# Performance work log

Measured on AMD Instinct MI355X. Metric: run time of the kernel, lower is better.

Reference implementation:

```python
import jax, jax.numpy as jnp
import numpy as np

B, N, D, H = 4, 4096, 1024, 16  # batch, seq_len, d_model, nhead
GN_EPS = 0.00064


def setup_inputs() -> dict:
    key = jax.random.key(0)
    ks = jax.random.split(key, 12)
    x = jax.random.normal(ks[0], (B, N, D), jnp.float32)
    ddd = jnp.linspace(0.0, 1.0, D).reshape(1, 1, D)
    s = 1.0 / np.sqrt(D)  # xavier-ish scale for DxD linears
    w = lambda k: jax.random.normal(k, (D, D), jnp.float32) * s
    return {
        "x": x,
        "x_r": 1.0 - ddd ** 0.2,
        "x_w": 1.0 - ddd ** 0.9,
        "x_k": 1.0 - ddd ** 0.7,
        "x_v": 1.0 - ddd ** 0.7,
        "x_a": 1.0 - ddd ** 0.9,
        "x_g": 1.0 - ddd ** 0.2,
        "W_r": w(ks[1]),   # receptance
        "W_w": w(ks[2]),   # time_decay
        "W_k": w(ks[3]),   # key
        "W_v": w(ks[4]),   # value
        "W_a": w(ks[5]),   # in_context
        "W_g": w(ks[6]),   # gate
        "W_out": jax.random.normal(ks[7], (D, D), jnp.float32) * s,
        "b_out": jax.random.normal(ks[8], (D,), jnp.float32) * 0.01,
        "gn_w": 1.0 + 0.1 * jax.random.normal(ks[9], (D,), jnp.float32),
        "gn_b": 0.1 * jax.random.normal(ks[10], (D,), jnp.float32),
    }


def reference(x, x_r, x_w, x_k, x_v, x_a, x_g,
              W_r, W_w, W_k, W_v, W_a, W_g,
              W_out, b_out, gn_w, gn_b):
    b, n, d = x.shape
    # previous-token shift delta: prev - x, with zero prev at t=0
    prev = jnp.concatenate([jnp.zeros_like(x[:, :1]), x[:, :-1]], axis=1)
    xx = prev - x

    lin = lambda mix, W: (x + xx * mix) @ W.T  # torch Linear: y = z @ W^T
    r = jax.nn.sigmoid(lin(x_r, W_r))
    decay = jnp.exp(-jax.nn.softplus(lin(x_w, W_w)))
    k = jnp.tanh(lin(x_k, W_k))
    v = lin(x_v, W_v)
    alpha = jax.nn.sigmoid(lin(x_a, W_a))
    g = jax.nn.sigmoid(lin(x_g, W_g))

    # per-channel recurrence: state = state * decay_t + alpha_t * k_t * v_t
    u = alpha * k * v  # [B, N, D]
    def step(state, inp):
        d_t, u_t, r_t = inp
        state = state * d_t + u_t
        return state, r_t * state

    inputs_tm = (jnp.swapaxes(decay, 0, 1),  # time-major [N, B, D]
                 jnp.swapaxes(u, 0, 1),
                 jnp.swapaxes(r, 0, 1))
    state0 = jnp.zeros((b, d), x.dtype)
    _, mixed_tm = jax.lax.scan(step, state0, inputs_tm)
    mixed = jnp.swapaxes(mixed_tm, 0, 1)  # [B, N, D]

    # GroupNorm(H groups) over reshaped [B*N, D]
    m = mixed.reshape(b * n, H, d // H)
    mu = m.mean(-1, keepdims=True)
    var = ((m - mu) ** 2).mean(-1, keepdims=True)  # biased, as torch GroupNorm
    mn = ((m - mu) / jnp.sqrt(var + GN_EPS)).reshape(b, n, d)
    mn = mn * gn_w + gn_b

    return (mn * g) @ W_out.T + b_out
```

## Files before the change

kernel.cpp:

```cpp
#include <hip/hip_runtime.h>
#include <cstdint>
#include <cstddef>

#define D_MODEL 1024
#define SEQ_LEN 4096
#define NBATCH  4
#define M_ROWS  (NBATCH * SEQ_LEN)
#define NCHUNK  64
#define CHLEN   64
#define GN_EPS_F 0.00064f

typedef unsigned short u16;
typedef __attribute__((ext_vector_type(4))) float f32x4;
typedef __attribute__((ext_vector_type(8))) __bf16 bf16x8;

enum { ACT_DECAY = 0, ACT_TANH, ACT_VMUL, ACT_U, ACT_SIG, ACT_BIAS, ACT_ID };

__device__ __forceinline__ u16 f2bf(float f) {
  union { float f; uint32_t u; } un; un.f = f;
  uint32_t r = (un.u + 0x7FFFu + ((un.u >> 16) & 1u)) >> 16;
  return (u16)r;
}
__device__ __forceinline__ float bf2f(u16 h) {
  union { uint32_t u; float f; } un; un.u = ((uint32_t)h) << 16;
  return un.f;
}
__device__ __forceinline__ float sigm(float y) { return 1.f / (1.f + expf(-y)); }

__device__ __forceinline__ void load_lds16(const u16* g, u16* l) {
  __builtin_amdgcn_global_load_lds(
      (const __attribute__((address_space(1))) void*)g,
      (__attribute__((address_space(3))) void*)l, 16, 0, 0);
}

__global__ __launch_bounds__(256) void wconv(
    const float* __restrict__ w0, const float* __restrict__ w1,
    const float* __restrict__ w2, const float* __restrict__ w3,
    const float* __restrict__ w4, const float* __restrict__ w5,
    const float* __restrict__ w6, u16* __restrict__ Wb) {
  const int gid = blockIdx.x * 256 + threadIdx.x;
  const int m = gid >> 18;
  const int off = gid & 262143;
  const float* src;
  switch (m) {
    case 0: src = w0; break; case 1: src = w1; break; case 2: src = w2; break;
    case 3: src = w3; break; case 4: src = w4; break; case 5: src = w5; break;
    default: src = w6; break;
  }
  const float4 v = ((const float4*)src)[off];
  ushort4 o;
  o.x = f2bf(v.x); o.y = f2bf(v.y); o.z = f2bf(v.z); o.w = f2bf(v.w);
  ((ushort4*)Wb)[gid] = o;
}

__global__ __launch_bounds__(256) void zgen2(
    const float* __restrict__ x, const float* __restrict__ mixA,
    const float* __restrict__ mixB, u16* __restrict__ zA,
    u16* __restrict__ zB) {
  const int gid = blockIdx.x * 256 + threadIdx.x;
  const int dv = gid & 255;
  const int n = (gid >> 8) & (SEQ_LEN - 1);
  const float4 xv = ((const float4*)x)[gid];
  float4 pv = make_float4(0.f, 0.f, 0.f, 0.f);
  if (n > 0) pv = ((const float4*)x)[gid - 256];
  const float4 dxv = make_float4(pv.x - xv.x, pv.y - xv.y, pv.z - xv.z, pv.w - xv.w);
  const float4 ma = ((const float4*)mixA)[dv];
  const float4 mb = ((const float4*)mixB)[dv];
  ushort4 oa, ob;
  oa.x = f2bf(xv.x + dxv.x * ma.x); ob.x = f2bf(xv.x + dxv.x * mb.x);
  oa.y = f2bf(xv.y + dxv.y * ma.y); ob.y = f2bf(xv.y + dxv.y * mb.y);
  oa.z = f2bf(xv.z + dxv.z * ma.z); ob.z = f2bf(xv.z + dxv.z * mb.z);
  oa.w = f2bf(xv.w + dxv.w * ma.w); ob.w = f2bf(xv.w + dxv.w * mb.w);
  ((ushort4*)zA)[gid] = oa;
  ((ushort4*)zB)[gid] = ob;
}

template <int ACT>
__global__ __launch_bounds__(512, 4) void gemm_bt(
    const u16* __restrict__ A,
    const u16* __restrict__ Bw,
    void* __restrict__ outp,
    const u16* __restrict__ aux,
    const float* __restrict__ bias) {
  __shared__ __align__(16) u16 AL[2][128 * 32];
  __shared__ __align__(16) u16 BL[2][256 * 32];
  const int tid = threadIdx.x;
  const int lane = tid & 63;
  const int wid = tid >> 6;
  const int wr = wid >> 2;
  const int wc = wid & 3;
  const int lr = lane & 15;
  const int lk = lane >> 4;

  const int bid = blockIdx.x;
  const int wgid = (bid & 7) * 64 + (bid >> 3);
  const int m0 = (wgid >> 2) * 128;
  const int n0 = (wgid & 3) * 256;

  const int srow = tid >> 2;
  const int ssw  = ((tid & 3) ^ ((srow >> 1) & 3)) * 8;
  const u16* gA  = A  + (size_t)(m0 + srow) * D_MODEL + ssw;
  const u16* gB0 = Bw + (size_t)(n0 + srow) * D_MODEL + ssw;
  const u16* gB1 = Bw + (size_t)(n0 + 128 + srow) * D_MODEL + ssw;
#define SA(bufi, kt) load_lds16(gA  + (kt), &AL[bufi][wid * 512])
#define SB0(bufi, kt) load_lds16(gB0 + (kt), &BL[bufi][wid * 512])
#define SB1(bufi, kt) load_lds16(gB1 + (kt), &BL[bufi][4096 + wid * 512])

  const int rA = wr * 64;
  const int rB = wc * 64;

  f32x4 acc[4][4];
  const f32x4 z4 = {0.f, 0.f, 0.f, 0.f};
#pragma unroll
  for (int i = 0; i < 4; i++)
#pragma unroll
    for (int j = 0; j < 4; j++) acc[i][j] = z4;

  SB0(0, 0); SB1(0, 0); SA(0, 0);

  int cur = 0;
  for (int t = 0; t < 32; ++t) {
    const int nxt = cur ^ 1;
    const int ktn = (t + 1) * 32;
    const bool more = (t < 31);
    const u16* uA = AL[cur];
    const u16* uB = BL[cur];
    bf16x8 a[4], b[4];

    if (more) { SB0(nxt, ktn); SB1(nxt, ktn); }
    if (more) asm volatile("s_waitcnt vmcnt(2)" ::: "memory");
    else      asm volatile("s_waitcnt vmcnt(0)" ::: "memory");
    __builtin_amdgcn_s_barrier();
    __builtin_amdgcn_sched_barrier(0);
#pragma unroll
    for (int mi = 0; mi < 4; ++mi) {
      const int R = rA + mi * 16 + lr;
      a[mi] = *(const bf16x8*)&uA[R * 32 + ((lk ^ ((R >> 1) & 3)) << 3)];
    }
#pragma unroll
    for (int nj = 0; nj < 4; ++nj) {
      const int R = rB + nj * 16 + lr;
      b[nj] = *(const bf16x8*)&uB[R * 32 + ((lk ^ ((R >> 1) & 3)) << 3)];
    }
    __builtin_amdgcn_s_setprio(1);
#pragma unroll
    for (int mi = 0; mi < 4; ++mi)
#pragma unroll
      for (int nj = 0; nj < 2; ++nj)
        acc[mi][nj] = __builtin_amdgcn_mfma_f32_16x16x32_bf16(a[mi], b[nj], acc[mi][nj], 0, 0, 0);
    __builtin_amdgcn_s_setprio(0);

    if (more) SA(nxt, ktn);
    __builtin_amdgcn_s_barrier();
    __builtin_amdgcn_s_setprio(1);
#pragma unroll
    for (int mi = 0; mi < 4; ++mi)
#pragma unroll
      for (int nj = 2; nj < 4; ++nj)
        acc[mi][nj] = __builtin_amdgcn_mfma_f32_16x16x32_bf16(a[mi], b[nj], acc[mi][nj], 0, 0, 0);
    __builtin_amdgcn_s_setprio(0);
    cur = nxt;
  }
#undef SA
#undef SB0
#undef SB1

#pragma unroll
  for (int mi = 0; mi < 4; ++mi) {
#pragma unroll
    for (int nj = 0; nj < 4; ++nj) {
#pragma unroll
      for (int e = 0; e < 4; ++e) {
        const int row = m0 + wr * 64 + mi * 16 + lk * 4 + e;
        const int col = n0 + wc * 64 + nj * 16 + lr;
        const size_t idx = (size_t)row * D_MODEL + col;
        const float y = acc[mi][nj][e];
        if constexpr (ACT == ACT_ID) {
          ((u16*)outp)[idx] = f2bf(y);
        } else if constexpr (ACT == ACT_TANH) {
          ((u16*)outp)[idx] = f2bf(tanhf(y));
        } else if constexpr (ACT == ACT_VMUL) {
          ((u16*)outp)[idx] = f2bf(y * bf2f(aux[idx]));
        } else if constexpr (ACT == ACT_U) {
          ((u16*)outp)[idx] = f2bf(sigm(y) * bf2f(aux[idx]));
        } else if constexpr (ACT == ACT_SIG) {
          ((u16*)outp)[idx] = f2bf(sigm(y));
        } else {
          ((float*)outp)[idx] = y + bias[col];
        }
      }
    }
  }
}

__global__ __launch_bounds__(256) void scan1(
    const u16* __restrict__ wraw, const u16* __restrict__ u,
    float* __restrict__ Ac, float* __restrict__ Sc) {
  const int gid = blockIdx.x * 256 + threadIdx.x;
  const int d = gid & 1023;
  const int b = (gid >> 10) & 3;
  const int c = gid >> 12;
  const size_t base = ((size_t)b * SEQ_LEN + (size_t)c * CHLEN) * D_MODEL + d;
  float A = 1.f, S = 0.f;
#pragma unroll 4
  for (int t = 0; t < CHLEN; t++) {
    const size_t off = base + (size_t)t * D_MODEL;
    const float dd = 1.f / (1.f + expf(bf2f(wraw[off])));
    S = S * dd + bf2f(u[off]);
    A *= dd;
  }
  Ac[gid] = A;
  Sc[gid] = S;
}

__global__ __launch_bounds__(256) void scan2(
    const float* __restrict__ Ac, const float* __restrict__ Sc,
    float* __restrict__ In) {
  const int gid = blockIdx.x * 256 + threadIdx.x;
  float carry = 0.f;
#pragma unroll 4
  for (int c = 0; c < NCHUNK; c++) {
    const int i = c * 4096 + gid;
    In[i] = carry;
    carry = carry * Ac[i] + Sc[i];
  }
}

__global__ __launch_bounds__(1024) void scan3gn(
    const u16* __restrict__ wraw, const u16* __restrict__ u,
    const u16* __restrict__ r, const u16* __restrict__ g,
    const float* __restrict__ In, const float* __restrict__ gw,
    const float* __restrict__ gb, u16* __restrict__ h) {
  const int d = threadIdx.x;
  const int b = blockIdx.x >> 6;
  const int c = blockIdx.x & 63;
  const size_t base = ((size_t)b * SEQ_LEN + (size_t)c * CHLEN) * D_MODEL + d;
  float state = In[c * 4096 + b * 1024 + d];
  const float w_ = gw[d], bb_ = gb[d];
  for (int t = 0; t < CHLEN; t++) {
    const size_t off = base + (size_t)t * D_MODEL;
    const float dd = 1.f / (1.f + expf(bf2f(wraw[off])));
    state = state * dd + bf2f(u[off]);
    const float mixed = bf2f(r[off]) * state;
    float s = mixed, s2 = mixed * mixed;
#pragma unroll
    for (int m = 32; m > 0; m >>= 1) {
      s += __shfl_xor(s, m, 64);
      s2 += __shfl_xor(s2, m, 64);
    }
    const float mu = s * (1.f / 64.f);
    const float var = s2 * (1.f / 64.f) - mu * mu;
    const float inv = 1.f / sqrtf(var + GN_EPS_F);
    h[off] = f2bf(((mixed - mu) * inv * w_ + bb_) * bf2f(g[off]));
  }
}

extern "C" void kernel_launch(void* const* d_in, const int* in_sizes, int n_in,
                              void* d_out, int out_size, void* d_ws, size_t ws_size,
                              hipStream_t stream) {
  (void)in_sizes; (void)n_in; (void)out_size; (void)ws_size;
  const float* x    = (const float*)d_in[0];
  const float* mx_r = (const float*)d_in[1];
  const float* mx_w = (const float*)d_in[2];
  const float* mx_k = (const float*)d_in[3];
  const float* mx_v = (const float*)d_in[4];
  const float* mx_a = (const float*)d_in[5];
  const float* mx_g = (const float*)d_in[6];
  const float* W_r  = (const float*)d_in[7];
  const float* W_w  = (const float*)d_in[8];
  const float* W_k  = (const float*)d_in[9];
  const float* W_v  = (const float*)d_in[10];
  const float* W_a  = (const float*)d_in[11];
  const float* W_g  = (const float*)d_in[12];
  const float* W_o  = (const float*)d_in[13];
  const float* b_out = (const float*)d_in[14];
  const float* gn_w  = (const float*)d_in[15];
  const float* gn_b  = (const float*)d_in[16];

  char* ws = (char*)d_ws;
  const size_t MB = 1024ull * 1024ull;
  u16*   Wb   = (u16*)(ws);
  float* Ac   = (float*)(ws + 14 * MB);
  float* Sc   = (float*)(ws + 15 * MB);
  u16*   z1   = (u16*)(ws + 16 * MB);
  u16*   z2   = (u16*)(ws + 48 * MB);
  u16*   wraw = (u16*)(ws + 80 * MB);
  u16*   ubuf = (u16*)(ws + 112 * MB);
  u16*   kbuf = (u16*)(ws + 144 * MB);
  u16*   vbuf = (u16*)(ws + 176 * MB);
  float* Inb  = (float*)(ws + 208 * MB);

  wconv<<<7168, 256, 0, stream>>>(W_r, W_w, W_k, W_v, W_a, W_g, W_o, Wb);

  zgen2<<<16384, 256, 0, stream>>>(x, mx_w, mx_k, z1, z2);
  gemm_bt<ACT_ID><<<512, 512, 0, stream>>>(z1, Wb + 1 * 1048576, wraw, nullptr, nullptr);
  gemm_bt<ACT_TANH><<<512, 512, 0, stream>>>(z2, Wb + 2 * 1048576, kbuf, nullptr, nullptr);
  zgen2<<<16384, 256, 0, stream>>>(x, mx_v, mx_a, z1, z2);
  gemm_bt<ACT_VMUL><<<512, 512, 0, stream>>>(z1, Wb + 3 * 1048576, vbuf, kbuf, nullptr);
  gemm_bt<ACT_U><<<512, 512, 0, stream>>>(z2, Wb + 4 * 1048576, ubuf, vbuf, nullptr);
  zgen2<<<16384, 256, 0, stream>>>(x, mx_r, mx_g, z1, z2);
  gemm_bt<ACT_SIG><<<512, 512, 0, stream>>>(z1, Wb + 0, kbuf, nullptr, nullptr);
  gemm_bt<ACT_SIG><<<512, 512, 0, stream>>>(z2, Wb + 5 * 1048576, vbuf, nullptr, nullptr);

  scan1<<<1024, 256, 0, stream>>>(wraw, ubuf, Ac, Sc);
  scan2<<<16, 256, 0, stream>>>(Ac, Sc, Inb);
  scan3gn<<<256, 1024, 0, stream>>>(wraw, ubuf, kbuf, vbuf, Inb, gn_w, gn_b, z2);

  gemm_bt<ACT_BIAS><<<512, 512, 0, stream>>>(z2, Wb + 6 * 1048576, (float*)d_out, nullptr, b_out);
}
```

Measured before the change: 497.4 us.

## Fold token-shift mixing into weights and batch projections into wide K=2048 GEMMs

The token-shift mix is folded into the weights algebraically: (x + (prev-x)*m) @ W^T becomes [x, prev] @ [W*(1-m); W*m]^T with K=2048, so the per-projection zgen passes go away and a single bf16 copy of x is read, with the previous row addressed through an offset (a zero page covers t=0). The six projections are merged into two GEMM launches with wider N grids and per-column-block epilogues, and a separate elementwise pass computes u=a*k*v. The scan and GroupNorm are split into separate kernels. The cost is twice the K work per projection, plus an extra bf16 round trip for the mixed tensor and the u pass.

New measurement: 651.7 us. 1.31x slower.

```diff
diff --git a/kernel.cpp b/kernel.cpp
--- a/kernel.cpp
+++ b/kernel.cpp
@@ -14,8 +14,6 @@
 typedef __attribute__((ext_vector_type(4))) float f32x4;
 typedef __attribute__((ext_vector_type(8))) __bf16 bf16x8;
 
-enum { ACT_DECAY = 0, ACT_TANH, ACT_VMUL, ACT_U, ACT_SIG, ACT_BIAS, ACT_ID };
-
 __device__ __forceinline__ u16 f2bf(float f) {
   union { float f; uint32_t u; } un; un.f = f;
   uint32_t r = (un.u + 0x7FFFu + ((un.u >> 16) & 1u)) >> 16;
@@ -33,55 +31,72 @@
       (__attribute__((address_space(3))) void*)l, 16, 0, 0);
 }
 
-__global__ __launch_bounds__(256) void wconv(
-    const float* __restrict__ w0, const float* __restrict__ w1,
-    const float* __restrict__ w2, const float* __restrict__ w3,
-    const float* __restrict__ w4, const float* __restrict__ w5,
-    const float* __restrict__ w6, u16* __restrict__ Wb) {
-  const int gid = blockIdx.x * 256 + threadIdx.x;
-  const int m = gid >> 18;
-  const int off = gid & 262143;
-  const float* src;
-  switch (m) {
-    case 0: src = w0; break; case 1: src = w1; break; case 2: src = w2; break;
-    case 3: src = w3; break; case 4: src = w4; break; case 5: src = w5; break;
-    default: src = w6; break;
-  }
-  const float4 v = ((const float4*)src)[off];
+__global__ __launch_bounds__(1024) void zset(u16* __restrict__ z) {
+  ((unsigned long long*)z)[threadIdx.x] = 0ull;
+}
+
+__global__ __launch_bounds__(256) void xgen(
+    const float* __restrict__ x, u16* __restrict__ xb) {
+  const int gid = blockIdx.x * 256 + threadIdx.x;
+  const float4 v0 = ((const float4*)x)[gid * 2];
+  const float4 v1 = ((const float4*)x)[gid * 2 + 1];
+  ushort4 o0, o1;
+  o0.x = f2bf(v0.x); o0.y = f2bf(v0.y); o0.z = f2bf(v0.z); o0.w = f2bf(v0.w);
+  o1.x = f2bf(v1.x); o1.y = f2bf(v1.y); o1.z = f2bf(v1.z); o1.w = f2bf(v1.w);
+  ((ushort4*)xb)[gid * 2] = o0;
+  ((ushort4*)xb)[gid * 2 + 1] = o1;
+}
+
+__global__ __launch_bounds__(256) void wconv2(
+    const float* __restrict__ Ww, const float* __restrict__ Wk,
+    const float* __restrict__ Wv, const float* __restrict__ Wa,
+    const float* __restrict__ Wr, const float* __restrict__ Wg,
+    const float* __restrict__ mw, const float* __restrict__ mk,
+    const float* __restrict__ mv, const float* __restrict__ ma,
+    const float* __restrict__ mr, const float* __restrict__ mg,
+    u16* __restrict__ Wall) {
+  const int gid = blockIdx.x * 256 + threadIdx.x;
+  const int p = gid >> 18;
+  const int rem = gid & 262143;
+  const int j = rem >> 8;
+  const int cv = rem & 255;
+  const float* W; const float* m;
+  switch (p) {
+    case 0: W = Ww; m = mw; break; case 1: W = Wk; m = mk; break;
+    case 2: W = Wv; m = mv; break; case 3: W = Wa; m = ma; break;
+    case 4: W = Wr; m = mr; break; default: W = Wg; m = mg; break;
+  }
+  const float4 w4 = ((const float4*)W)[j * 256 + cv];
+  const float4 m4 = ((const float4*)m)[cv];
+  ushort4 lo, hi;
+  lo.x = f2bf(w4.x * (1.f - m4.x)); hi.x = f2bf(w4.x * m4.x);
+  lo.y = f2bf(w4.y * (1.f - m4.y)); hi.y = f2bf(w4.y * m4.y);
+  lo.z = f2bf(w4.z * (1.f - m4.z)); hi.z = f2bf(w4.z * m4.z);
+  lo.w = f2bf(w4.w * (1.f - m4.w)); hi.w = f2bf(w4.w * m4.w);
+  u16* rowp = Wall + (size_t)(p * 1024 + j) * 2048;
+  ((ushort4*)rowp)[cv] = lo;
+  ((ushort4*)(rowp + 1024))[cv] = hi;
+}
+
+__global__ __launch_bounds__(256) void wconvO(
+    const float* __restrict__ W, u16* __restrict__ Wb) {
+  const int gid = blockIdx.x * 256 + threadIdx.x;
+  const float4 v = ((const float4*)W)[gid];
   ushort4 o;
   o.x = f2bf(v.x); o.y = f2bf(v.y); o.z = f2bf(v.z); o.w = f2bf(v.w);
   ((ushort4*)Wb)[gid] = o;
 }
 
-__global__ __launch_bounds__(256) void zgen2(
-    const float* __restrict__ x, const float* __restrict__ mixA,
-    const float* __restrict__ mixB, u16* __restrict__ zA,
-    u16* __restrict__ zB) {
-  const int gid = blockIdx.x * 256 + threadIdx.x;
-  const int dv = gid & 255;
-  const int n = (gid >> 8) & (SEQ_LEN - 1);
-  const float4 xv = ((const float4*)x)[gid];
-  float4 pv = make_float4(0.f, 0.f, 0.f, 0.f);
-  if (n > 0) pv = ((const float4*)x)[gid - 256];
-  const float4 dxv = make_float4(pv.x - xv.x, pv.y - xv.y, pv.z - xv.z, pv.w - xv.w);
-  const float4 ma = ((const float4*)mixA)[dv];
-  const float4 mb = ((const float4*)mixB)[dv];
-  ushort4 oa, ob;
-  oa.x = f2bf(xv.x + dxv.x * ma.x); ob.x = f2bf(xv.x + dxv.x * mb.x);
-  oa.y = f2bf(xv.y + dxv.y * ma.y); ob.y = f2bf(xv.y + dxv.y * mb.y);
-  oa.z = f2bf(xv.z + dxv.z * ma.z); ob.z = f2bf(xv.z + dxv.z * mb.z);
-  oa.w = f2bf(xv.w + dxv.w * ma.w); ob.w = f2bf(xv.w + dxv.w * mb.w);
-  ((ushort4*)zA)[gid] = oa;
-  ((ushort4*)zB)[gid] = ob;
-}
-
-template <int ACT>
+template <int MODE, int KDIM, int NT>
 __global__ __launch_bounds__(512, 4) void gemm_bt(
     const u16* __restrict__ A,
     const u16* __restrict__ Bw,
-    void* __restrict__ outp,
-    const u16* __restrict__ aux,
-    const float* __restrict__ bias) {
+    const u16* __restrict__ zpage,
+    u16* __restrict__ o0, u16* __restrict__ o1,
+    u16* __restrict__ o2, u16* __restrict__ o3,
+    float* __restrict__ fout, const float* __restrict__ bias) {
+  constexpr int NK = KDIM / 32;
+  constexpr int GRID = (M_ROWS / 128) * NT;
   __shared__ __align__(16) u16 AL[2][128 * 32];
   __shared__ __align__(16) u16 BL[2][256 * 32];
   const int tid = threadIdx.x;
@@ -93,18 +108,19 @@
   const int lk = lane >> 4;
 
   const int bid = blockIdx.x;
-  const int wgid = (bid & 7) * 64 + (bid >> 3);
-  const int m0 = (wgid >> 2) * 128;
-  const int n0 = (wgid & 3) * 256;
+  const int logical = (bid & 7) * (GRID / 8) + (bid >> 3);
+  const int m0 = (logical / NT) * 128;
+  const int n0 = (logical % NT) * 256;
 
   const int srow = tid >> 2;
   const int ssw  = ((tid & 3) ^ ((srow >> 1) & 3)) * 8;
-  const u16* gA  = A  + (size_t)(m0 + srow) * D_MODEL + ssw;
-  const u16* gB0 = Bw + (size_t)(n0 + srow) * D_MODEL + ssw;
-  const u16* gB1 = Bw + (size_t)(n0 + 128 + srow) * D_MODEL + ssw;
-#define SA(bufi, kt) load_lds16(gA  + (kt), &AL[bufi][wid * 512])
-#define SB0(bufi, kt) load_lds16(gB0 + (kt), &BL[bufi][wid * 512])
-#define SB1(bufi, kt) load_lds16(gB1 + (kt), &BL[bufi][4096 + wid * 512])
+  const int arow = m0 + srow;
+  const u16* gA_lo = A + (size_t)arow * 1024 + ssw;
+  const u16* gA_hi = ((arow & (SEQ_LEN - 1)) == 0)
+                         ? (zpage + ssw)
+                         : (A + (size_t)(arow - 1) * 1024 + ssw);
+  const u16* gB0 = Bw + (size_t)(n0 + srow) * KDIM + ssw;
+  const u16* gB1 = Bw + (size_t)(n0 + 128 + srow) * KDIM + ssw;
 
   const int rA = wr * 64;
   const int rB = wc * 64;
@@ -116,20 +132,26 @@
 #pragma unroll
     for (int j = 0; j < 4; j++) acc[i][j] = z4;
 
-  SB0(0, 0); SB1(0, 0); SA(0, 0);
+  load_lds16(gB0, &BL[0][wid * 512]);
+  load_lds16(gB1, &BL[0][4096 + wid * 512]);
+  load_lds16(gA_lo, &AL[0][wid * 512]);
 
   int cur = 0;
-  for (int t = 0; t < 32; ++t) {
+  for (int t = 0; t < NK; ++t) {
     const int nxt = cur ^ 1;
     const int ktn = (t + 1) * 32;
-    const bool more = (t < 31);
+    const bool more = (t < NK - 1);
     const u16* uA = AL[cur];
     const u16* uB = BL[cur];
     bf16x8 a[4], b[4];
 
-    if (more) { SB0(nxt, ktn); SB1(nxt, ktn); }
-    if (more) asm volatile("s_waitcnt vmcnt(2)" ::: "memory");
-    else      asm volatile("s_waitcnt vmcnt(0)" ::: "memory");
+    if (more) {
+      load_lds16(gB0 + ktn, &BL[nxt][wid * 512]);
+      load_lds16(gB1 + ktn, &BL[nxt][4096 + wid * 512]);
+      asm volatile("s_waitcnt vmcnt(2)" ::: "memory");
+    } else {
+      asm volatile("s_waitcnt vmcnt(0)" ::: "memory");
+    }
     __builtin_amdgcn_s_barrier();
     __builtin_amdgcn_sched_barrier(0);
 #pragma unroll
@@ -150,7 +172,11 @@
         acc[mi][nj] = __builtin_amdgcn_mfma_f32_16x16x32_bf16(a[mi], b[nj], acc[mi][nj], 0, 0, 0);
     __builtin_amdgcn_s_setprio(0);
 
-    if (more) SA(nxt, ktn);
+    if (more) {
+      const u16* sA = (KDIM == 2048 && ktn >= 1024) ? gA_hi + (ktn - 1024)
+                                                    : gA_lo + ktn;
+      load_lds16(sA, &AL[nxt][wid * 512]);
+    }
     __builtin_amdgcn_s_barrier();
     __builtin_amdgcn_s_setprio(1);
 #pragma unroll
@@ -161,10 +187,8 @@
     __builtin_amdgcn_s_setprio(0);
     cur = nxt;
   }
-#undef SA
-#undef SB0
-#undef SB1
-
+
+  const int p = n0 >> 10;
 #pragma unroll
   for (int mi = 0; mi < 4; ++mi) {
 #pragma unroll
@@ -172,25 +196,46 @@
 #pragma unroll
       for (int e = 0; e < 4; ++e) {
         const int row = m0 + wr * 64 + mi * 16 + lk * 4 + e;
-        const int col = n0 + wc * 64 + nj * 16 + lr;
+        const int colg = n0 + wc * 64 + nj * 16 + lr;
+        const int col = colg & 1023;
         const size_t idx = (size_t)row * D_MODEL + col;
         const float y = acc[mi][nj][e];
-        if constexpr (ACT == ACT_ID) {
-          ((u16*)outp)[idx] = f2bf(y);
-        } else if constexpr (ACT == ACT_TANH) {
-          ((u16*)outp)[idx] = f2bf(tanhf(y));
-        } else if constexpr (ACT == ACT_VMUL) {
-          ((u16*)outp)[idx] = f2bf(y * bf2f(aux[idx]));
-        } else if constexpr (ACT == ACT_U) {
-          ((u16*)outp)[idx] = f2bf(sigm(y) * bf2f(aux[idx]));
-        } else if constexpr (ACT == ACT_SIG) {
-          ((u16*)outp)[idx] = f2bf(sigm(y));
+        if constexpr (MODE == 0) {
+          switch (p) {
+            case 0: o0[idx] = f2bf(y); break;
+            case 1: o1[idx] = f2bf(tanhf(y)); break;
+            case 2: o2[idx] = f2bf(y); break;
+            default: o3[idx] = f2bf(sigm(y)); break;
+          }
+        } else if constexpr (MODE == 1) {
+          if (p == 0) o0[idx] = f2bf(sigm(y));
+          else        o1[idx] = f2bf(sigm(y));
         } else {
-          ((float*)outp)[idx] = y + bias[col];
+          fout[idx] = y + bias[col];
         }
       }
     }
   }
+}
+
+__global__ __launch_bounds__(256) void upass(
+    u16* __restrict__ a, const u16* __restrict__ k,
+    const u16* __restrict__ v) {
+  const int gid = blockIdx.x * 256 + threadIdx.x;
+  uint4 av = ((const uint4*)a)[gid];
+  const uint4 kv = ((const uint4*)k)[gid];
+  const uint4 vv = ((const uint4*)v)[gid];
+  uint4 ov;
+  uint32_t* ap = (uint32_t*)&av; const uint32_t* kp = (const uint32_t*)&kv;
+  const uint32_t* vp = (const uint32_t*)&vv; uint32_t* op = (uint32_t*)&ov;
+#pragma unroll
+  for (int i = 0; i < 4; i++) {
+    const float a0 = bf2f((u16)(ap[i] & 0xFFFF)), a1 = bf2f((u16)(ap[i] >> 16));
+    const float k0 = bf2f((u16)(kp[i] & 0xFFFF)), k1 = bf2f((u16)(kp[i] >> 16));
+    const float v0 = bf2f((u16)(vp[i] & 0xFFFF)), v1 = bf2f((u16)(vp[i] >> 16));
+    op[i] = (uint32_t)f2bf(a0 * k0 * v0) | ((uint32_t)f2bf(a1 * k1 * v1) << 16);
+  }
+  ((uint4*)a)[gid] = ov;
 }
 
 __global__ __launch_bounds__(256) void scan1(
@@ -226,33 +271,48 @@
   }
 }
 
-__global__ __launch_bounds__(1024) void scan3gn(
+__global__ __launch_bounds__(256) void scan3(
     const u16* __restrict__ wraw, const u16* __restrict__ u,
-    const u16* __restrict__ r, const u16* __restrict__ g,
-    const float* __restrict__ In, const float* __restrict__ gw,
-    const float* __restrict__ gb, u16* __restrict__ h) {
-  const int d = threadIdx.x;
-  const int b = blockIdx.x >> 6;
-  const int c = blockIdx.x & 63;
+    const u16* __restrict__ r, const float* __restrict__ In,
+    u16* __restrict__ mixed) {
+  const int gid = blockIdx.x * 256 + threadIdx.x;
+  const int d = gid & 1023;
+  const int b = (gid >> 10) & 3;
+  const int c = gid >> 12;
   const size_t base = ((size_t)b * SEQ_LEN + (size_t)c * CHLEN) * D_MODEL + d;
-  float state = In[c * 4096 + b * 1024 + d];
-  const float w_ = gw[d], bb_ = gb[d];
+  float state = In[gid];
+#pragma unroll 4
   for (int t = 0; t < CHLEN; t++) {
     const size_t off = base + (size_t)t * D_MODEL;
     const float dd = 1.f / (1.f + expf(bf2f(wraw[off])));
     state = state * dd + bf2f(u[off]);
-    const float mixed = bf2f(r[off]) * state;
-    float s = mixed, s2 = mixed * mixed;
-#pragma unroll
-    for (int m = 32; m > 0; m >>= 1) {
-      s += __shfl_xor(s, m, 64);
-      s2 += __shfl_xor(s2, m, 64);
-    }
-    const float mu = s * (1.f / 64.f);
-    const float var = s2 * (1.f / 64.f) - mu * mu;
-    const float inv = 1.f / sqrtf(var + GN_EPS_F);
-    h[off] = f2bf(((mixed - mu) * inv * w_ + bb_) * bf2f(g[off]));
-  }
+    mixed[off] = f2bf(bf2f(r[off]) * state);
+  }
+}
+
+__global__ __launch_bounds__(256) void gnorm(
+    const u16* __restrict__ mixed, const u16* __restrict__ g,
+    const float* __restrict__ gw, const float* __restrict__ gb,
+    u16* __restrict__ h) {
+  const int wid = threadIdx.x >> 6;
+  const int lane = threadIdx.x & 63;
+  const int grp = blockIdx.x * 4 + wid;
+  const int row = grp >> 4;
+  const int hh = grp & 15;
+  const int d = hh * 64 + lane;
+  const size_t idx = (size_t)row * D_MODEL + d;
+  const float v = bf2f(mixed[idx]);
+  float s = v, s2 = v * v;
+#pragma unroll
+  for (int m = 32; m > 0; m >>= 1) {
+    s += __shfl_xor(s, m, 64);
+    s2 += __shfl_xor(s2, m, 64);
+  }
+  const float mu = s * (1.f / 64.f);
+  const float var = s2 * (1.f / 64.f) - mu * mu;
+  const float inv = 1.f / sqrtf(var + GN_EPS_F);
+  const float mn = (v - mu) * inv * gw[d] + gb[d];
+  h[idx] = f2bf(mn * bf2f(g[idx]));
 }
 
 extern "C" void kernel_launch(void* const* d_in, const int* in_sizes, int n_in,
@@ -279,32 +339,38 @@
 
   char* ws = (char*)d_ws;
   const size_t MB = 1024ull * 1024ull;
-  u16*   Wb   = (u16*)(ws);
-  float* Ac   = (float*)(ws + 14 * MB);
-  float* Sc   = (float*)(ws + 15 * MB);
-  u16*   z1   = (u16*)(ws + 16 * MB);
-  u16*   z2   = (u16*)(ws + 48 * MB);
-  u16*   wraw = (u16*)(ws + 80 * MB);
-  u16*   ubuf = (u16*)(ws + 112 * MB);
-  u16*   kbuf = (u16*)(ws + 144 * MB);
-  u16*   vbuf = (u16*)(ws + 176 * MB);
-  float* Inb  = (float*)(ws + 208 * MB);
-
-  wconv<<<7168, 256, 0, stream>>>(W_r, W_w, W_k, W_v, W_a, W_g, W_o, Wb);
-
-  zgen2<<<16384, 256, 0, stream>>>(x, mx_w, mx_k, z1, z2);
-  gemm_bt<ACT_ID><<<512, 512, 0, stream>>>(z1, Wb + 1 * 1048576, wraw, nullptr, nullptr);
-  gemm_bt<ACT_TANH><<<512, 512, 0, stream>>>(z2, Wb + 2 * 1048576, kbuf, nullptr, nullptr);
-  zgen2<<<16384, 256, 0, stream>>>(x, mx_v, mx_a, z1, z2);
-  gemm_bt<ACT_VMUL><<<512, 512, 0, stream>>>(z1, Wb + 3 * 1048576, vbuf, kbuf, nullptr);
-  gemm_bt<ACT_U><<<512, 512, 0, stream>>>(z2, Wb + 4 * 1048576, ubuf, vbuf, nullptr);
-  zgen2<<<16384, 256, 0, stream>>>(x, mx_r, mx_g, z1, z2);
-  gemm_bt<ACT_SIG><<<512, 512, 0, stream>>>(z1, Wb + 0, kbuf, nullptr, nullptr);
-  gemm_bt<ACT_SIG><<<512, 512, 0, stream>>>(z2, Wb + 5 * 1048576, vbuf, nullptr, nullptr);
-
-  scan1<<<1024, 256, 0, stream>>>(wraw, ubuf, Ac, Sc);
+  u16*   Wall  = (u16*)(ws);
+  u16*   Woutb = (u16*)(ws + 24 * MB);
+  float* Ac    = (float*)(ws + 26 * MB);
+  float* Sc    = (float*)(ws + 27 * MB);
+  float* Inb   = (float*)(ws + 28 * MB);
+  u16*   zpage = (u16*)(ws + 29 * MB);
+  u16*   xbf   = (u16*)(ws + 32 * MB);
+  u16*   wraw  = (u16*)(ws + 64 * MB);
+  u16*   kbuf  = (u16*)(ws + 96 * MB);
+  u16*   vbuf  = (u16*)(ws + 128 * MB);
+  u16*   abuf  = (u16*)(ws + 160 * MB);
+
+  zset<<<1, 1024, 0, stream>>>(zpage);
+  wconv2<<<6144, 256, 0, stream>>>(W_w, W_k, W_v, W_a, W_r, W_g,
+                                   mx_w, mx_k, mx_v, mx_a, mx_r, mx_g, Wall);
+  wconvO<<<1024, 256, 0, stream>>>(W_o, Woutb);
+  xgen<<<8192, 256, 0, stream>>>(x, xbf);
+
+  gemm_bt<0, 2048, 16><<<2048, 512, 0, stream>>>(
+      xbf, Wall, zpage, wraw, kbuf, vbuf, abuf, nullptr, nullptr);
+  upass<<<8192, 256, 0, stream>>>(abuf, kbuf, vbuf);
+  gemm_bt<1, 2048, 8><<<1024, 512, 0, stream>>>(
+      xbf, Wall + (size_t)4096 * 2048, zpage, kbuf, vbuf, nullptr, nullptr,
+      nullptr, nullptr);
+
+  scan1<<<1024, 256, 0, stream>>>(wraw, abuf, Ac, Sc);
   scan2<<<16, 256, 0, stream>>>(Ac, Sc, Inb);
-  scan3gn<<<256, 1024, 0, stream>>>(wraw, ubuf, kbuf, vbuf, Inb, gn_w, gn_b, z2);
-
-  gemm_bt<ACT_BIAS><<<512, 512, 0, stream>>>(z2, Wb + 6 * 1048576, (float*)d_out, nullptr, b_out);
-}
+  scan3<<<1024, 256, 0, stream>>>(wraw, abuf, kbuf, Inb, xbf);
+
+  gnorm<<<65536, 256, 0, stream>>>(xbf, vbuf, gn_w, gn_b, kbuf);
+
+  gemm_bt<2, 1024, 4><<<512, 512, 0, stream>>>(
+      kbuf, Woutb, zpage, nullptr, nullptr, nullptr, nullptr,
+      (float*)d_out, b_out);
+}
```

## Vectorize chunked scan eight channels per thread and split group norm into separate kernel

Applied to the files above, without the earlier changes.

scan1 and the chunk-apply scan now have each thread handle 8 channels using 16-byte loads, so far fewer threads run (128 blocks of 256). The group norm is moved out of the scan into its own fully parallel kernel that reads the bf16 mixed buffer and does an 8-lane shuffle reduction. The aim is wider memory transactions and removing the per-timestep 64-lane shuffle from the serial loop. The cost is an extra write and read of the mixed tensor, and fewer threads in the scan kernels, which risks lower occupancy and less latency hiding.

Result: slower. 606.9 us (+22.0%).

```diff
diff --git a/kernel.cpp b/kernel.cpp
--- a/kernel.cpp
+++ b/kernel.cpp
@@ -26,6 +26,22 @@
   return un.f;
 }
 __device__ __forceinline__ float sigm(float y) { return 1.f / (1.f + expf(-y)); }
+
+__device__ __forceinline__ void unp8(const uint4 v, float* f) {
+  const uint32_t* p = (const uint32_t*)&v;
+#pragma unroll
+  for (int i = 0; i < 4; i++) {
+    f[2 * i]     = bf2f((u16)(p[i] & 0xFFFF));
+    f[2 * i + 1] = bf2f((u16)(p[i] >> 16));
+  }
+}
+__device__ __forceinline__ uint4 pck8(const float* f) {
+  uint4 v; uint32_t* p = (uint32_t*)&v;
+#pragma unroll
+  for (int i = 0; i < 4; i++)
+    p[i] = (uint32_t)f2bf(f[2 * i]) | ((uint32_t)f2bf(f[2 * i + 1]) << 16);
+  return v;
+}
 
 __device__ __forceinline__ void load_lds16(const u16* g, u16* l) {
   __builtin_amdgcn_global_load_lds(
@@ -197,20 +213,32 @@
     const u16* __restrict__ wraw, const u16* __restrict__ u,
     float* __restrict__ Ac, float* __restrict__ Sc) {
   const int gid = blockIdx.x * 256 + threadIdx.x;
-  const int d = gid & 1023;
-  const int b = (gid >> 10) & 3;
-  const int c = gid >> 12;
-  const size_t base = ((size_t)b * SEQ_LEN + (size_t)c * CHLEN) * D_MODEL + d;
-  float A = 1.f, S = 0.f;
-#pragma unroll 4
-  for (int t = 0; t < CHLEN; t++) {
-    const size_t off = base + (size_t)t * D_MODEL;
-    const float dd = 1.f / (1.f + expf(bf2f(wraw[off])));
-    S = S * dd + bf2f(u[off]);
-    A *= dd;
-  }
-  Ac[gid] = A;
-  Sc[gid] = S;
+  const int dv = gid & 127;
+  const int b = (gid >> 7) & 3;
+  const int c = gid >> 9;
+  const uint4* w4 = (const uint4*)wraw;
+  const uint4* u4 = (const uint4*)u;
+  size_t off = ((size_t)b * SEQ_LEN + (size_t)c * CHLEN) * 128 + dv;
+  float A[8], S[8];
+#pragma unroll
+  for (int i = 0; i < 8; i++) { A[i] = 1.f; S[i] = 0.f; }
+#pragma unroll 2
+  for (int t = 0; t < CHLEN; t++, off += 128) {
+    float wv[8], uv[8];
+    unp8(w4[off], wv);
+    unp8(u4[off], uv);
+#pragma unroll
+    for (int i = 0; i < 8; i++) {
+      const float dd = 1.f / (1.f + expf(wv[i]));
+      S[i] = S[i] * dd + uv[i];
+      A[i] *= dd;
+    }
+  }
+  const int o4 = c * 1024 + b * 256 + dv * 2;
+  ((float4*)Ac)[o4]     = make_float4(A[0], A[1], A[2], A[3]);
+  ((float4*)Ac)[o4 + 1] = make_float4(A[4], A[5], A[6], A[7]);
+  ((float4*)Sc)[o4]     = make_float4(S[0], S[1], S[2], S[3]);
+  ((float4*)Sc)[o4 + 1] = make_float4(S[4], S[5], S[6], S[7]);
 }
 
 __global__ __launch_bounds__(256) void scan2(
@@ -226,33 +254,72 @@
   }
 }
 
-__global__ __launch_bounds__(1024) void scan3gn(
+__global__ __launch_bounds__(256) void scan3(
     const u16* __restrict__ wraw, const u16* __restrict__ u,
-    const u16* __restrict__ r, const u16* __restrict__ g,
-    const float* __restrict__ In, const float* __restrict__ gw,
-    const float* __restrict__ gb, u16* __restrict__ h) {
-  const int d = threadIdx.x;
-  const int b = blockIdx.x >> 6;
-  const int c = blockIdx.x & 63;
-  const size_t base = ((size_t)b * SEQ_LEN + (size_t)c * CHLEN) * D_MODEL + d;
-  float state = In[c * 4096 + b * 1024 + d];
-  const float w_ = gw[d], bb_ = gb[d];
-  for (int t = 0; t < CHLEN; t++) {
-    const size_t off = base + (size_t)t * D_MODEL;
-    const float dd = 1.f / (1.f + expf(bf2f(wraw[off])));
-    state = state * dd + bf2f(u[off]);
-    const float mixed = bf2f(r[off]) * state;
-    float s = mixed, s2 = mixed * mixed;
-#pragma unroll
-    for (int m = 32; m > 0; m >>= 1) {
-      s += __shfl_xor(s, m, 64);
-      s2 += __shfl_xor(s2, m, 64);
-    }
-    const float mu = s * (1.f / 64.f);
-    const float var = s2 * (1.f / 64.f) - mu * mu;
-    const float inv = 1.f / sqrtf(var + GN_EPS_F);
-    h[off] = f2bf(((mixed - mu) * inv * w_ + bb_) * bf2f(g[off]));
-  }
+    const u16* __restrict__ r, const float* __restrict__ In,
+    u16* __restrict__ mixed) {
+  const int gid = blockIdx.x * 256 + threadIdx.x;
+  const int dv = gid & 127;
+  const int b = (gid >> 7) & 3;
+  const int c = gid >> 9;
+  const uint4* w4 = (const uint4*)wraw;
+  const uint4* u4 = (const uint4*)u;
+  const uint4* r4 = (const uint4*)r;
+  uint4* m4 = (uint4*)mixed;
+  size_t off = ((size_t)b * SEQ_LEN + (size_t)c * CHLEN) * 128 + dv;
+  const int o4 = c * 1024 + b * 256 + dv * 2;
+  const float4 s0 = ((const float4*)In)[o4];
+  const float4 s1 = ((const float4*)In)[o4 + 1];
+  float S[8] = {s0.x, s0.y, s0.z, s0.w, s1.x, s1.y, s1.z, s1.w};
+#pragma unroll 2
+  for (int t = 0; t < CHLEN; t++, off += 128) {
+    float wv[8], uv[8], rv[8], mv[8];
+    unp8(w4[off], wv);
+    unp8(u4[off], uv);
+    unp8(r4[off], rv);
+#pragma unroll
+    for (int i = 0; i < 8; i++) {
+      const float dd = 1.f / (1.f + expf(wv[i]));
+      S[i] = S[i] * dd + uv[i];
+      mv[i] = rv[i] * S[i];
+    }
+    m4[off] = pck8(mv);
+  }
+}
+
+__global__ __launch_bounds__(256) void gnorm(
+    const u16* __restrict__ mixed, const u16* __restrict__ g,
+    const float* __restrict__ gw, const float* __restrict__ gb,
+    u16* __restrict__ h) {
+  const int G = blockIdx.x * 32 + (threadIdx.x >> 3);
+  const int sub = threadIdx.x & 7;
+  const int row = G >> 4;
+  const int hh = G & 15;
+  const int d0 = hh * 64 + sub * 8;
+  const size_t i4 = ((size_t)row * D_MODEL + d0) >> 3;
+  float mv[8], gv[8];
+  unp8(((const uint4*)mixed)[i4], mv);
+  unp8(((const uint4*)g)[i4], gv);
+  float s = 0.f, s2 = 0.f;
+#pragma unroll
+  for (int i = 0; i < 8; i++) { s += mv[i]; s2 += mv[i] * mv[i]; }
+#pragma unroll
+  for (int m = 1; m < 8; m <<= 1) {
+    s += __shfl_xor(s, m, 64);
+    s2 += __shfl_xor(s2, m, 64);
+  }
+  const float mu = s * (1.f / 64.f);
+  const float var = s2 * (1.f / 64.f) - mu * mu;
+  const float inv = 1.f / sqrtf(var + GN_EPS_F);
+  const float4 gw0 = ((const float4*)gw)[d0 >> 2], gw1 = ((const float4*)gw)[(d0 >> 2) + 1];
+  const float4 gb0 = ((const float4*)gb)[d0 >> 2], gb1 = ((const float4*)gb)[(d0 >> 2) + 1];
+  const float W[8] = {gw0.x, gw0.y, gw0.z, gw0.w, gw1.x, gw1.y, gw1.z, gw1.w};
+  const float Bb[8] = {gb0.x, gb0.y, gb0.z, gb0.w, gb1.x, gb1.y, gb1.z, gb1.w};
+  float ov[8];
+#pragma unroll
+  for (int i = 0; i < 8; i++)
+    ov[i] = ((mv[i] - mu) * inv * W[i] + Bb[i]) * gv[i];
+  ((uint4*)h)[i4] = pck8(ov);
 }
 
 extern "C" void kernel_launch(void* const* d_in, const int* in_sizes, int n_in,
@@ -302,9 +369,11 @@
   gemm_bt<ACT_SIG><<<512, 512, 0, stream>>>(z1, Wb + 0, kbuf, nullptr, nullptr);
   gemm_bt<ACT_SIG><<<512, 512, 0, stream>>>(z2, Wb + 5 * 1048576, vbuf, nullptr, nullptr);
 
-  scan1<<<1024, 256, 0, stream>>>(wraw, ubuf, Ac, Sc);
+  scan1<<<128, 256, 0, stream>>>(wraw, ubuf, Ac, Sc);
   scan2<<<16, 256, 0, stream>>>(Ac, Sc, Inb);
-  scan3gn<<<256, 1024, 0, stream>>>(wraw, ubuf, kbuf, vbuf, Inb, gn_w, gn_b, z2);
+  scan3<<<128, 256, 0, stream>>>(wraw, ubuf, kbuf, Inb, z1);
+
+  gnorm<<<8192, 256, 0, stream>>>(z1, vbuf, gn_w, gn_b, z2);
 
   gemm_bt<ACT_BIAS><<<512, 512, 0, stream>>>(z2, Wb + 6 * 1048576, (float*)d_out, nullptr, b_out);
 }
```

## Split scan3 and GroupNorm into separate kernels with vectorized group-norm pass

Applied to the files above, without the earlier changes.

The fused scan-and-GroupNorm kernel (256 blocks of 1024 threads, one shuffle reduction per timestep) becomes two kernels. A scan kernel with 1024 blocks of 256 threads writes the mixed values to a bf16 buffer. A separate GroupNorm kernel then uses 8 threads per group, each with 16-byte vector loads and stores. This takes the per-step shuffle reductions off the serial scan's critical path and gives more blocks, at the cost of an extra write and read of the mixed tensor plus one more launch.

Measured after the change: 478.6 us. 1.04x faster.

```diff
diff --git a/kernel.cpp b/kernel.cpp
--- a/kernel.cpp
+++ b/kernel.cpp
@@ -26,6 +26,22 @@
   return un.f;
 }
 __device__ __forceinline__ float sigm(float y) { return 1.f / (1.f + expf(-y)); }
+
+__device__ __forceinline__ void unp8(const uint4 v, float* f) {
+  const uint32_t* p = (const uint32_t*)&v;
+#pragma unroll
+  for (int i = 0; i < 4; i++) {
+    f[2 * i]     = bf2f((u16)(p[i] & 0xFFFF));
+    f[2 * i + 1] = bf2f((u16)(p[i] >> 16));
+  }
+}
+__device__ __forceinline__ uint4 pck8(const float* f) {
+  uint4 v; uint32_t* p = (uint32_t*)&v;
+#pragma unroll
+  for (int i = 0; i < 4; i++)
+    p[i] = (uint32_t)f2bf(f[2 * i]) | ((uint32_t)f2bf(f[2 * i + 1]) << 16);
+  return v;
+}
 
 __device__ __forceinline__ void load_lds16(const u16* g, u16* l) {
   __builtin_amdgcn_global_load_lds(
@@ -226,33 +242,58 @@
   }
 }
 
-__global__ __launch_bounds__(1024) void scan3gn(
+__global__ __launch_bounds__(256) void scan3(
     const u16* __restrict__ wraw, const u16* __restrict__ u,
-    const u16* __restrict__ r, const u16* __restrict__ g,
-    const float* __restrict__ In, const float* __restrict__ gw,
-    const float* __restrict__ gb, u16* __restrict__ h) {
-  const int d = threadIdx.x;
-  const int b = blockIdx.x >> 6;
-  const int c = blockIdx.x & 63;
+    const u16* __restrict__ r, const float* __restrict__ In,
+    u16* __restrict__ mixed) {
+  const int gid = blockIdx.x * 256 + threadIdx.x;
+  const int d = gid & 1023;
+  const int b = (gid >> 10) & 3;
+  const int c = gid >> 12;
   const size_t base = ((size_t)b * SEQ_LEN + (size_t)c * CHLEN) * D_MODEL + d;
-  float state = In[c * 4096 + b * 1024 + d];
-  const float w_ = gw[d], bb_ = gb[d];
+  float state = In[gid];
+#pragma unroll 4
   for (int t = 0; t < CHLEN; t++) {
     const size_t off = base + (size_t)t * D_MODEL;
     const float dd = 1.f / (1.f + expf(bf2f(wraw[off])));
     state = state * dd + bf2f(u[off]);
-    const float mixed = bf2f(r[off]) * state;
-    float s = mixed, s2 = mixed * mixed;
-#pragma unroll
-    for (int m = 32; m > 0; m >>= 1) {
-      s += __shfl_xor(s, m, 64);
-      s2 += __shfl_xor(s2, m, 64);
-    }
-    const float mu = s * (1.f / 64.f);
-    const float var = s2 * (1.f / 64.f) - mu * mu;
-    const float inv = 1.f / sqrtf(var + GN_EPS_F);
-    h[off] = f2bf(((mixed - mu) * inv * w_ + bb_) * bf2f(g[off]));
-  }
+    mixed[off] = f2bf(bf2f(r[off]) * state);
+  }
+}
+
+__global__ __launch_bounds__(256) void gnorm(
+    const u16* __restrict__ mixed, const u16* __restrict__ g,
+    const float* __restrict__ gw, const float* __restrict__ gb,
+    u16* __restrict__ h) {
+  const int G = blockIdx.x * 32 + (threadIdx.x >> 3);
+  const int sub = threadIdx.x & 7;
+  const int row = G >> 4;
+  const int hh = G & 15;
+  const int d0 = hh * 64 + sub * 8;
+  const size_t i4 = ((size_t)row * D_MODEL + d0) >> 3;
+  float mv[8], gv[8];
+  unp8(((const uint4*)mixed)[i4], mv);
+  unp8(((const uint4*)g)[i4], gv);
+  float s = 0.f, s2 = 0.f;
+#pragma unroll
+  for (int i = 0; i < 8; i++) { s += mv[i]; s2 += mv[i] * mv[i]; }
+#pragma unroll
+  for (int m = 1; m < 8; m <<= 1) {
+    s += __shfl_xor(s, m, 64);
+    s2 += __shfl_xor(s2, m, 64);
+  }
+  const float mu = s * (1.f / 64.f);
+  const float var = s2 * (1.f / 64.f) - mu * mu;
+  const float inv = 1.f / sqrtf(var + GN_EPS_F);
+  const float4 gw0 = ((const float4*)gw)[d0 >> 2], gw1 = ((const float4*)gw)[(d0 >> 2) + 1];
+  const float4 gb0 = ((const float4*)gb)[d0 >> 2], gb1 = ((const float4*)gb)[(d0 >> 2) + 1];
+  const float W[8] = {gw0.x, gw0.y, gw0.z, gw0.w, gw1.x, gw1.y, gw1.z, gw1.w};
+  const float Bb[8] = {gb0.x, gb0.y, gb0.z, gb0.w, gb1.x, gb1.y, gb1.z, gb1.w};
+  float ov[8];
+#pragma unroll
+  for (int i = 0; i < 8; i++)
+    ov[i] = ((mv[i] - mu) * inv * W[i] + Bb[i]) * gv[i];
+  ((uint4*)h)[i4] = pck8(ov);
 }
 
 extern "C" void kernel_launch(void* const* d_in, const int* in_sizes, int n_in,
@@ -304,7 +345,9 @@
 
   scan1<<<1024, 256, 0, stream>>>(wraw, ubuf, Ac, Sc);
   scan2<<<16, 256, 0, stream>>>(Ac, Sc, Inb);
-  scan3gn<<<256, 1024, 0, stream>>>(wraw, ubuf, kbuf, vbuf, Inb, gn_w, gn_b, z2);
+  scan3<<<1024, 256, 0, stream>>>(wraw, ubuf, kbuf, Inb, z1);
+
+  gnorm<<<8192, 256, 0, stream>>>(z1, vbuf, gn_w, gn_b, z2);
 
   gemm_bt<ACT_BIAS><<<512, 512, 0, stream>>>(z2, Wb + 6 * 1048576, (float*)d_out, nullptr, b_out);
 }
```
